# Performance work log

Hardware: AMD Instinct MI355X
Metric: run time of the kernel (lower is better)

Reference implementation:

```python
import jax, jax.numpy as jnp
import numpy as np

INPUT_DIM = 21
HIDDEN = 512
OUT_DIM = 20


def _lstm_cell(xt, h, c, Wx, bx, Wh):
    # xt: (B, in), h/c: (B, H); Wx: (4H, in), Wh: (4H, H), bx: (4H,)
    gates = xt @ Wx.T + bx + h @ Wh.T          # (B, 4H)
    i, f, g, o = jnp.split(gates, 4, axis=-1)   # torch chunk order: i, f, g, o
    i = jax.nn.sigmoid(i)
    f = jax.nn.sigmoid(f)
    g = jnp.tanh(g)
    o = jax.nn.sigmoid(o)
    c_new = f * c + i * g
    h_new = o * jnp.tanh(c_new)
    return h_new, c_new


def setup_inputs() -> dict:
    key = jax.random.key(0)
    ks = jax.random.split(key, 8)
    s_in = 1.0 / np.sqrt(INPUT_DIM)
    s_h = 1.0 / np.sqrt(HIDDEN)
    x = jax.random.normal(ks[0], (64, 1024, INPUT_DIM), dtype=jnp.float32)
    Wx0 = jax.random.uniform(ks[1], (4 * HIDDEN, INPUT_DIM), jnp.float32, -s_in, s_in)
    bx0 = jax.random.uniform(ks[2], (4 * HIDDEN,), jnp.float32, -s_in, s_in)
    Wh0 = jax.random.uniform(ks[3], (4 * HIDDEN, HIDDEN), jnp.float32, -s_h, s_h)
    Wx1 = jax.random.uniform(ks[4], (4 * HIDDEN, HIDDEN), jnp.float32, -s_h, s_h)
    bx1 = jax.random.uniform(ks[5], (4 * HIDDEN,), jnp.float32, -s_h, s_h)
    Wh1 = jax.random.uniform(ks[6], (4 * HIDDEN, HIDDEN), jnp.float32, -s_h, s_h)
    Wo = jax.random.uniform(ks[7], (OUT_DIM, HIDDEN), jnp.float32, -s_h, s_h)
    bo = jnp.zeros((OUT_DIM,), jnp.float32)
    return {"x": x, "Wx0": Wx0, "bx0": bx0, "Wh0": Wh0,
            "Wx1": Wx1, "bx1": bx1, "Wh1": Wh1, "Wo": Wo, "bo": bo}


def reference(x, Wx0, bx0, Wh0, Wx1, bx1, Wh1, Wo, bo):
    B, T, _ = x.shape
    H = Wh0.shape[1]
    h0 = jnp.zeros((B, H), x.dtype)
    c0 = jnp.zeros((B, H), x.dtype)
    h1 = jnp.zeros((B, H), x.dtype)
    c1 = jnp.zeros((B, H), x.dtype)

    def step(carry, xt):
        h0, c0, h1, c1 = carry
        h0, c0 = _lstm_cell(xt, h0, c0, Wx0, bx0, Wh0)
        h1, c1 = _lstm_cell(h0, h1, c1, Wx1, bx1, Wh1)
        out = jax.nn.sigmoid(h1 @ Wo.T + bo)  # (B, OUT_DIM)
        return (h0, c0, h1, c1), out

    _, outs = jax.lax.scan(step, (h0, c0, h1, c1), jnp.swapaxes(x, 0, 1))
    return jnp.swapaxes(outs, 0, 1)  # (B, T, OUT_DIM)
```

## Files before the change

### kernel.cpp

```cpp
#include <hip/hip_runtime.h>


#define T_STEPS 1024
#define WS_FLAG_OFF 0
#define WS_H0_OFF  4096
#define WS_H1_OFF  (4096 + 8*4*8192)
#define WS_NEED    (WS_H1_OFF + 8*2*8192)

#define SCOPE __HIP_MEMORY_SCOPE_AGENT

typedef _Float16 f16;
typedef _Float16 f16x8 __attribute__((ext_vector_type(8)));
typedef float    f32x4 __attribute__((ext_vector_type(4)));
typedef unsigned long long u64;

#define HP_STRIDE 520

__device__ __forceinline__ float sigm_(float x) {
    x = fminf(fmaxf(x, -30.f), 30.f);
    return 1.f / (1.f + __expf(-x));
}
__device__ __forceinline__ float tanh_(float x) {
    x = fminf(fmaxf(x, -15.f), 15.f);
    float e = __expf(-2.f * x);
    return (1.f - e) / (1.f + e);
}

__device__ __forceinline__ f16x8 afrag_lds(const f16* __restrict__ hp, int kbase,
                                           int b, int q) {
    return *(const f16x8*)(hp + (b & 7) * HP_STRIDE + kbase + q * 8);
}

__device__ __forceinline__ f16x8 pack8(const float* p) {
    float4 a = *(const float4*)p, b = *(const float4*)(p + 4);
    f16x8 f;
    f[0] = (f16)a.x; f[1] = (f16)a.y; f[2] = (f16)a.z; f[3] = (f16)a.w;
    f[4] = (f16)b.x; f[5] = (f16)b.y; f[6] = (f16)b.z; f[7] = (f16)b.w;
    return f;
}

__device__ __forceinline__ long long wait_flags(const int* f0, int t0,
                                                const int* f1, int t1, int lane,
                                                long long predict_clk) {
    const int* p = (lane & 16) ? (f1 + (lane & 15) * 4) : (f0 + (lane & 15) * 4);
    const int tgt = (lane & 16) ? t1 : t0;
    const bool act = (lane < 32);
    int v = act ? __hip_atomic_load(p, __ATOMIC_RELAXED, SCOPE) : 0x7fffffff;
    if (__all(v >= tgt)) return 0;
    long long t0c = (long long)__builtin_amdgcn_s_memtime();
    int rep = (int)(predict_clk >> 12);
    if (rep > 8) rep = 8;
    for (int i = 0; i < rep; ++i) __builtin_amdgcn_s_sleep(31);
    int spins = 0;
    for (;;) {
        v = act ? __hip_atomic_load(p, __ATOMIC_RELAXED, SCOPE) : 0x7fffffff;
        if (__all(v >= tgt)) break;
        ++spins;
        if (spins < 32)       __builtin_amdgcn_s_sleep(1);
        else if (spins < 256) __builtin_amdgcn_s_sleep(4);
        else                  __builtin_amdgcn_s_sleep(16);
        if (spins > (1 << 20)) break;
    }
    return (long long)__builtin_amdgcn_s_memtime() - t0c;
}

__device__ __forceinline__ long long ewma_upd(long long ew, long long d) {
    return ew - (ew >> 2) + (d >> 2);
}

__device__ __forceinline__ u64 ld8_sc0(const u64* p) {
    u64 v;
    asm volatile("global_load_dwordx2 %0, %1, off sc0" : "=v"(v) : "v"(p));
    return v;
}

__device__ __forceinline__ void stage_plane(const f16* __restrict__ gp,
                                            f16* __restrict__ dst, int tid,
                                            bool fast) {
    const u64* g8 = (const u64*)gp;
    u64 v[4];
    if (fast) {
#pragma unroll
        for (int jj = 0; jj < 4; ++jj) v[jj] = ld8_sc0(g8 + jj * 256 + tid);
        asm volatile("s_waitcnt vmcnt(0)" ::: "memory");
    } else {
#pragma unroll
        for (int jj = 0; jj < 4; ++jj)
            v[jj] = __hip_atomic_load(g8 + jj * 256 + tid, __ATOMIC_RELAXED, SCOPE);
    }
#pragma unroll
    for (int jj = 0; jj < 4; ++jj) {
        int i = jj * 256 + tid;
        int wg = i >> 6, b = (i >> 3) & 7, j = i & 7;
        *(u64*)(dst + b * HP_STRIDE + wg * 32 + j * 4) = v[jj];
    }
}

__device__ __forceinline__ void stage_two(const f16* __restrict__ gpA,
                                          f16* __restrict__ dstA,
                                          const f16* __restrict__ gpB,
                                          f16* __restrict__ dstB, int tid,
                                          bool fast) {
    const u64* ga = (const u64*)gpA;
    const u64* gb = (const u64*)gpB;
    u64 va[4], vb[4];
    if (fast) {
#pragma unroll
        for (int jj = 0; jj < 4; ++jj) va[jj] = ld8_sc0(ga + jj * 256 + tid);
#pragma unroll
        for (int jj = 0; jj < 4; ++jj) vb[jj] = ld8_sc0(gb + jj * 256 + tid);
        asm volatile("s_waitcnt vmcnt(0)" ::: "memory");
    } else {
#pragma unroll
        for (int jj = 0; jj < 4; ++jj)
            va[jj] = __hip_atomic_load(ga + jj * 256 + tid, __ATOMIC_RELAXED, SCOPE);
#pragma unroll
        for (int jj = 0; jj < 4; ++jj)
            vb[jj] = __hip_atomic_load(gb + jj * 256 + tid, __ATOMIC_RELAXED, SCOPE);
    }
#pragma unroll
    for (int jj = 0; jj < 4; ++jj) {
        int i = jj * 256 + tid;
        int wg = i >> 6, b = (i >> 3) & 7, j = i & 7;
        *(u64*)(dstA + b * HP_STRIDE + wg * 32 + j * 4) = va[jj];
        *(u64*)(dstB + b * HP_STRIDE + wg * 32 + j * 4) = vb[jj];
    }
}

__device__ __forceinline__ f16x8 load_xfrag(const float* __restrict__ x,
                                            int gb8, int t, int ln, int q) {
    f16x8 f = {(_Float16)0, (_Float16)0, (_Float16)0, (_Float16)0,
               (_Float16)0, (_Float16)0, (_Float16)0, (_Float16)0};
    if (ln < 8 && t < T_STEPS) {
        const float* xp = x + ((size_t)(gb8 + ln) * 1024 + t) * 21;
#pragma unroll
        for (int j = 0; j < 8; ++j) {
            int kl = q * 8 + j;
            if (kl < 21) f[j] = (f16)xp[kl];
        }
    }
    return f;
}

__global__ void zero_ws_kernel(unsigned* __restrict__ p, int ndw) {
    int i = blockIdx.x * blockDim.x + threadIdx.x;
    int stride = gridDim.x * blockDim.x;
    for (; i < ndw; i += stride)
        __hip_atomic_store(p + i, 0u, __ATOMIC_RELAXED, SCOPE);
}

__global__ __launch_bounds__(256, 1)
void lstm_persist(const float* __restrict__ x,
                  const float* __restrict__ Wx0, const float* __restrict__ bx0,
                  const float* __restrict__ Wh0,
                  const float* __restrict__ Wx1, const float* __restrict__ bx1,
                  const float* __restrict__ Wh1,
                  const float* __restrict__ Wo,  const float* __restrict__ bo,
                  float* __restrict__ out, char* __restrict__ ws) {
    struct SM {
        float g[4][8][33];
        float c[8][32];
        float bias[4][32];
        __align__(8)  f16 hout[8][32];
        __align__(16) f16 planeA[8 * HP_STRIDE];
        __align__(16) f16 planeB[8 * HP_STRIDE];
        char  pad[60 * 1024];
    };
    __shared__ SM sm;
    __shared__ int s_fast;
    const int tid = threadIdx.x;
    if (tid == 0x00FFFFFFu) sm.pad[0] = 1;

    const int bid  = blockIdx.x;
    const int g    = bid & 7;
    const int rk   = bid >> 3;
    const int role = rk >> 4;
    const int r    = rk & 15;
    const int w    = tid >> 6;
    const int lane = tid & 63;
    const int ln   = lane & 15;
    const int q    = lane >> 4;
    const int gb8  = g * 8;

    int* barb  = (int*)(ws + WS_FLAG_OFF) + g * 128;
    int* flag0 = barb;
    int* flag1 = barb + 64;
    f16* H0g = (f16*)(ws + WS_H0_OFF) + g * 16384;
    f16* H1g = (f16*)(ws + WS_H1_OFF) + g * 8192;

    ((float*)sm.c)[tid] = 0.f;
    if (tid < 128) {
        int gate = tid >> 5, u = tid & 31;
        const float* bx = role ? bx1 : bx0;
        sm.bias[gate][u] = bx[(gate << 9) + (r << 5) + u];
    }

    f16x8 W[64];
    if (role == 0) {
#pragma unroll
        for (int tau = 0; tau < 2; ++tau) {
            const int rw = (w << 9) + (r << 5) + tau * 16 + ln;
            const float* wh0r = Wh0 + (size_t)rw * 512;
#pragma unroll
            for (int kk = 0; kk < 16; ++kk)
                W[tau * 17 + kk] = pack8(wh0r + kk * 32 + q * 8);
            const float* wx0r = Wx0 + (size_t)rw * 21;
            f16x8 f = {(_Float16)0, (_Float16)0, (_Float16)0, (_Float16)0,
                       (_Float16)0, (_Float16)0, (_Float16)0, (_Float16)0};
#pragma unroll
            for (int j = 0; j < 8; ++j) {
                int kl = q * 8 + j;
                if (kl < 21) f[j] = (f16)wx0r[kl];
            }
            W[tau * 17 + 16] = f;
        }
    } else {
#pragma unroll
        for (int tau = 0; tau < 2; ++tau) {
            const int rw = (w << 9) + (r << 5) + tau * 16 + ln;
            const float* wx1r = Wx1 + (size_t)rw * 512;
            const float* wh1r = Wh1 + (size_t)rw * 512;
#pragma unroll
            for (int kk = 0; kk < 16; ++kk)
                W[tau * 32 + kk] = pack8(wx1r + kk * 32 + q * 8);
#pragma unroll
            for (int kk = 16; kk < 32; ++kk)
                W[tau * 32 + kk] = pack8(wh1r + (kk - 16) * 32 + q * 8);
        }
    }

    if (tid == 0) {
        unsigned xcc;
        asm volatile("s_getreg_b32 %0, hwreg(HW_REG_XCC_ID)" : "=s"(xcc));
        __hip_atomic_fetch_or(barb + 1, (int)(1u << (xcc & 31)),
                              __ATOMIC_RELAXED, SCOPE);
        __hip_atomic_fetch_add(barb + 2, 1, __ATOMIC_RELAXED, SCOPE);
        int cnt = 0, spins = 0;
        for (;;) {
            cnt = __hip_atomic_load(barb + 2, __ATOMIC_RELAXED, SCOPE);
            if (cnt >= 32 || spins > (1 << 18)) break;
            __builtin_amdgcn_s_sleep(2);
            ++spins;
        }
        unsigned m = (unsigned)__hip_atomic_load(barb + 1, __ATOMIC_RELAXED, SCOPE);
        s_fast = (cnt >= 32 && __popc(m) == 1) ? 1 : 0;
    }
    __syncthreads();
    const bool fast = (s_fast != 0);

    if (role == 0) {
        long long ew = 0;
        for (int t = 0; t < T_STEPS; ++t) {
            const int wr = t & 3, rd = (t + 3) & 3;
            f16x8 xf = load_xfrag(x, gb8, t, ln, q);
            if (tid < 64) {
                long long d = wait_flags(flag0, t, flag1, t - 3, lane, ew);
                ew = ewma_upd(ew, d);
            }
            __syncthreads();
            stage_plane(H0g + rd * 4096, sm.planeA, tid, fast);
            __syncthreads();

            f32x4 a0 = {0, 0, 0, 0}, a1 = {0, 0, 0, 0};
#pragma unroll
            for (int kk = 0; kk < 16; ++kk) {
                f16x8 A = afrag_lds(sm.planeA, kk * 32, ln, q);
                a0 = __builtin_amdgcn_mfma_f32_16x16x32_f16(A, W[kk], a0, 0, 0, 0);
                a1 = __builtin_amdgcn_mfma_f32_16x16x32_f16(A, W[17 + kk], a1, 0, 0, 0);
            }
            a0 = __builtin_amdgcn_mfma_f32_16x16x32_f16(xf, W[16], a0, 0, 0, 0);
            a1 = __builtin_amdgcn_mfma_f32_16x16x32_f16(xf, W[33], a1, 0, 0, 0);
            if (q < 2) {
#pragma unroll
                for (int r4 = 0; r4 < 4; ++r4) {
                    sm.g[w][q * 4 + r4][ln] = a0[r4];
                    sm.g[w][q * 4 + r4][16 + ln] = a1[r4];
                }
            }
            __syncthreads();
            {
                int b = tid >> 5, u = tid & 31;
                float gi = sm.g[0][b][u] + sm.bias[0][u];
                float gf = sm.g[1][b][u] + sm.bias[1][u];
                float gg = sm.g[2][b][u] + sm.bias[2][u];
                float go = sm.g[3][b][u] + sm.bias[3][u];
                float iv = sigm_(gi), fv = sigm_(gf), gv = tanh_(gg), ov = sigm_(go);
                float c = sm.c[b][u];
                float cn = fv * c + iv * gv;
                sm.c[b][u] = cn;
                sm.hout[b][u] = (f16)(ov * tanh_(cn));
            }
            __syncthreads();
            if (tid < 64) {
                int b = tid >> 3, j = tid & 7;
                u64 v = *(const u64*)&sm.hout[b][j * 4];
                u64* dp = (u64*)(H0g + wr * 4096 + (r << 8) + (b << 5) + (j << 2));
                if (fast) *dp = v;
                else __hip_atomic_store(dp, v, __ATOMIC_RELAXED, SCOPE);
                asm volatile("s_waitcnt vmcnt(0)" ::: "memory");
                if (tid == 0)
                    __hip_atomic_store(flag0 + r * 4, t + 1, __ATOMIC_RELAXED, SCOPE);
            }
        }
    } else {
        long long ew = 0;
        for (int t = 0; t < T_STEPS; ++t) {
            const int wr = t & 1, rd = wr ^ 1;

            if (tid < 64) {
                long long d = wait_flags(flag0, t + 1, flag1, t, lane, ew);
                ew = ewma_upd(ew, d);
            }
            __syncthreads();
            stage_two(H0g + (t & 3) * 4096, sm.planeA,
                      H1g + rd * 4096,      sm.planeB,
                      tid, fast);
            __syncthreads();

            f32x4 a0 = {0, 0, 0, 0}, a1 = {0, 0, 0, 0};
#pragma unroll
            for (int kk = 0; kk < 16; ++kk) {
                f16x8 A = afrag_lds(sm.planeA, kk * 32, ln, q);
                a0 = __builtin_amdgcn_mfma_f32_16x16x32_f16(A, W[kk], a0, 0, 0, 0);
                a1 = __builtin_amdgcn_mfma_f32_16x16x32_f16(A, W[32 + kk], a1, 0, 0, 0);
            }
#pragma unroll
            for (int kk = 16; kk < 32; ++kk) {
                f16x8 A = afrag_lds(sm.planeB, (kk - 16) * 32, ln, q);
                a0 = __builtin_amdgcn_mfma_f32_16x16x32_f16(A, W[kk], a0, 0, 0, 0);
                a1 = __builtin_amdgcn_mfma_f32_16x16x32_f16(A, W[32 + kk], a1, 0, 0, 0);
            }
            if (q < 2) {
#pragma unroll
                for (int r4 = 0; r4 < 4; ++r4) {
                    sm.g[w][q * 4 + r4][ln] = a0[r4];
                    sm.g[w][q * 4 + r4][16 + ln] = a1[r4];
                }
            }
            __syncthreads();
            {
                int b = tid >> 5, u = tid & 31;
                float gi = sm.g[0][b][u] + sm.bias[0][u];
                float gf = sm.g[1][b][u] + sm.bias[1][u];
                float gg = sm.g[2][b][u] + sm.bias[2][u];
                float go = sm.g[3][b][u] + sm.bias[3][u];
                float iv = sigm_(gi), fv = sigm_(gf), gv = tanh_(gg), ov = sigm_(go);
                float c = sm.c[b][u];
                float cn = fv * c + iv * gv;
                sm.c[b][u] = cn;
                sm.hout[b][u] = (f16)(ov * tanh_(cn));
            }
            __syncthreads();
            if (tid < 64) {
                int b = tid >> 3, j = tid & 7;
                u64 v = *(const u64*)&sm.hout[b][j * 4];
                u64* dp = (u64*)(H1g + wr * 4096 + (r << 8) + (b << 5) + (j << 2));
                if (fast) *dp = v;
                else __hip_atomic_store(dp, v, __ATOMIC_RELAXED, SCOPE);
                asm volatile("s_waitcnt vmcnt(0)" ::: "memory");
                if (tid == 0)
                    __hip_atomic_store(flag1 + r * 4, t + 1, __ATOMIC_RELAXED, SCOPE);
            }

            if (t > 0) {
                int p = tid >> 4, kp = tid & 15;
                int valid = (p < 10);
                int idx = r * 10 + p;
                int b = valid ? idx / 20 : 0, o = valid ? idx % 20 : 0;
                float a = 0.f;
                if (valid) {
                    const f16* hp = sm.planeB + b * HP_STRIDE + kp * 32;
                    const float* wo = Wo + (size_t)o * 512 + kp * 32;
#pragma unroll
                    for (int k = 0; k < 32; k += 8) {
                        f16x8 hv = *(const f16x8*)(hp + k);
                        float4 wa = *(const float4*)(wo + k);
                        float4 wb = *(const float4*)(wo + k + 4);
                        a += (float)hv[0] * wa.x + (float)hv[1] * wa.y +
                             (float)hv[2] * wa.z + (float)hv[3] * wa.w +
                             (float)hv[4] * wb.x + (float)hv[5] * wb.y +
                             (float)hv[6] * wb.z + (float)hv[7] * wb.w;
                    }
                }
                a += __shfl_down(a, 8, 16);
                a += __shfl_down(a, 4, 16);
                a += __shfl_down(a, 2, 16);
                a += __shfl_down(a, 1, 16);
                if (valid && kp == 0)
                    out[((size_t)(gb8 + b) * 1024 + (t - 1)) * 20 + o] =
                        sigm_(a + bo[o]);
            }
        }

        if (tid < 64) wait_flags(flag1, T_STEPS, flag1, T_STEPS, lane, 0);
        __syncthreads();
        stage_plane(H1g + ((T_STEPS - 1) & 1) * 4096, sm.planeB, tid, fast);
        __syncthreads();
        {
            int p = tid >> 4, kp = tid & 15;
            int valid = (p < 10);
            int idx = r * 10 + p;
            int b = valid ? idx / 20 : 0, o = valid ? idx % 20 : 0;
            float a = 0.f;
            if (valid) {
                const f16* hp = sm.planeB + b * HP_STRIDE + kp * 32;
                const float* wo = Wo + (size_t)o * 512 + kp * 32;
#pragma unroll
                for (int k = 0; k < 32; k += 8) {
                    f16x8 hv = *(const f16x8*)(hp + k);
                    float4 wa = *(const float4*)(wo + k);
                    float4 wb = *(const float4*)(wo + k + 4);
                    a += (float)hv[0] * wa.x + (float)hv[1] * wa.y +
                         (float)hv[2] * wa.z + (float)hv[3] * wa.w +
                         (float)hv[4] * wb.x + (float)hv[5] * wb.y +
                         (float)hv[6] * wb.z + (float)hv[7] * wb.w;
                }
            }
            a += __shfl_down(a, 8, 16);
            a += __shfl_down(a, 4, 16);
            a += __shfl_down(a, 2, 16);
            a += __shfl_down(a, 1, 16);
            if (valid && kp == 0)
                out[((size_t)(gb8 + b) * 1024 + (T_STEPS - 1)) * 20 + o] =
                    sigm_(a + bo[o]);
        }
    }
}

extern "C" void kernel_launch(void* const* d_in, const int* in_sizes, int n_in,
                              void* d_out, int out_size, void* d_ws, size_t ws_size,
                              hipStream_t stream) {
    const float* x   = (const float*)d_in[0];
    const float* Wx0 = (const float*)d_in[1];
    const float* bx0 = (const float*)d_in[2];
    const float* Wh0 = (const float*)d_in[3];
    const float* Wx1 = (const float*)d_in[4];
    const float* bx1 = (const float*)d_in[5];
    const float* Wh1 = (const float*)d_in[6];
    const float* Wo  = (const float*)d_in[7];
    const float* bo  = (const float*)d_in[8];
    float* out = (float*)d_out;
    char*  ws  = (char*)d_ws;

    if (ws_size < (size_t)WS_NEED) return;

    zero_ws_kernel<<<128, 256, 0, stream>>>((unsigned*)ws, WS_NEED / 4);
    lstm_persist<<<256, 256, 0, stream>>>(x, Wx0, bx0, Wh0, Wx1, bx1, Wh1,
                                          Wo, bo, out, ws);
}
```

Baseline: 3.439 ms.

## Precompute layer-1 input projection for next step before waiting on h1

Splits the layer-1 step so the Wx1·h0 half of the gate GEMM for step t+1 is computed right after publishing h1 for step t, as soon as layer 0's h0 is ready. At step t+1 the layer-1 blocks then only wait for h1 and do the Wh1 half, which shortens the per-step critical path on the recurrent dependency. The cost is separate flag waits and staging for each plane, extra barriers, and accumulator registers carried across iterations.

```diff
diff --git a/kernel.cpp b/kernel.cpp
--- a/kernel.cpp
+++ b/kernel.cpp
@@ -8,6 +8,7 @@
 #define WS_NEED    (WS_H1_OFF + 8*2*8192)
 
 #define SCOPE __HIP_MEMORY_SCOPE_AGENT
+#define NEG_INF_T (-1000000000)
 
 typedef _Float16 f16;
 typedef _Float16 f16x8 __attribute__((ext_vector_type(8)));
@@ -96,37 +97,6 @@
     }
 }
 
-__device__ __forceinline__ void stage_two(const f16* __restrict__ gpA,
-                                          f16* __restrict__ dstA,
-                                          const f16* __restrict__ gpB,
-                                          f16* __restrict__ dstB, int tid,
-                                          bool fast) {
-    const u64* ga = (const u64*)gpA;
-    const u64* gb = (const u64*)gpB;
-    u64 va[4], vb[4];
-    if (fast) {
-#pragma unroll
-        for (int jj = 0; jj < 4; ++jj) va[jj] = ld8_sc0(ga + jj * 256 + tid);
-#pragma unroll
-        for (int jj = 0; jj < 4; ++jj) vb[jj] = ld8_sc0(gb + jj * 256 + tid);
-        asm volatile("s_waitcnt vmcnt(0)" ::: "memory");
-    } else {
-#pragma unroll
-        for (int jj = 0; jj < 4; ++jj)
-            va[jj] = __hip_atomic_load(ga + jj * 256 + tid, __ATOMIC_RELAXED, SCOPE);
-#pragma unroll
-        for (int jj = 0; jj < 4; ++jj)
-            vb[jj] = __hip_atomic_load(gb + jj * 256 + tid, __ATOMIC_RELAXED, SCOPE);
-    }
-#pragma unroll
-    for (int jj = 0; jj < 4; ++jj) {
-        int i = jj * 256 + tid;
-        int wg = i >> 6, b = (i >> 3) & 7, j = i & 7;
-        *(u64*)(dstA + b * HP_STRIDE + wg * 32 + j * 4) = va[jj];
-        *(u64*)(dstB + b * HP_STRIDE + wg * 32 + j * 4) = vb[jj];
-    }
-}
-
 __device__ __forceinline__ f16x8 load_xfrag(const float* __restrict__ x,
                                             int gb8, int t, int ln, int q) {
     f16x8 f = {(_Float16)0, (_Float16)0, (_Float16)0, (_Float16)0,
@@ -303,27 +273,32 @@
             }
         }
     } else {
-        long long ew = 0;
+        long long ew0 = 0, ew1 = 0;
+        f32x4 pA0 = {0, 0, 0, 0}, pA1 = {0, 0, 0, 0};
+
+        if (tid < 64) wait_flags(flag0, 1, flag1, NEG_INF_T, lane, 0);
+        __syncthreads();
+        stage_plane(H0g + 0 * 4096, sm.planeA, tid, fast);
+        __syncthreads();
+#pragma unroll
+        for (int kk = 0; kk < 16; ++kk) {
+            f16x8 A = afrag_lds(sm.planeA, kk * 32, ln, q);
+            pA0 = __builtin_amdgcn_mfma_f32_16x16x32_f16(A, W[kk], pA0, 0, 0, 0);
+            pA1 = __builtin_amdgcn_mfma_f32_16x16x32_f16(A, W[32 + kk], pA1, 0, 0, 0);
+        }
+
         for (int t = 0; t < T_STEPS; ++t) {
             const int wr = t & 1, rd = wr ^ 1;
 
             if (tid < 64) {
-                long long d = wait_flags(flag0, t + 1, flag1, t, lane, ew);
-                ew = ewma_upd(ew, d);
-            }
-            __syncthreads();
-            stage_two(H0g + (t & 3) * 4096, sm.planeA,
-                      H1g + rd * 4096,      sm.planeB,
-                      tid, fast);
-            __syncthreads();
-
-            f32x4 a0 = {0, 0, 0, 0}, a1 = {0, 0, 0, 0};
-#pragma unroll
-            for (int kk = 0; kk < 16; ++kk) {
-                f16x8 A = afrag_lds(sm.planeA, kk * 32, ln, q);
-                a0 = __builtin_amdgcn_mfma_f32_16x16x32_f16(A, W[kk], a0, 0, 0, 0);
-                a1 = __builtin_amdgcn_mfma_f32_16x16x32_f16(A, W[32 + kk], a1, 0, 0, 0);
-            }
+                long long d = wait_flags(flag1, t, flag1, t, lane, ew1);
+                ew1 = ewma_upd(ew1, d);
+            }
+            __syncthreads();
+            stage_plane(H1g + rd * 4096, sm.planeB, tid, fast);
+            __syncthreads();
+
+            f32x4 a0 = pA0, a1 = pA1;
 #pragma unroll
             for (int kk = 16; kk < 32; ++kk) {
                 f16x8 A = afrag_lds(sm.planeB, (kk - 16) * 32, ln, q);
@@ -360,6 +335,25 @@
                 asm volatile("s_waitcnt vmcnt(0)" ::: "memory");
                 if (tid == 0)
                     __hip_atomic_store(flag1 + r * 4, t + 1, __ATOMIC_RELAXED, SCOPE);
+            }
+
+            if (t + 1 < T_STEPS) {
+                if (tid < 64) {
+                    long long d = wait_flags(flag0, t + 2, flag1, NEG_INF_T,
+                                             lane, ew0);
+                    ew0 = ewma_upd(ew0, d);
+                }
+                __syncthreads();
+                stage_plane(H0g + ((t + 1) & 3) * 4096, sm.planeA, tid, fast);
+                __syncthreads();
+                pA0 = (f32x4){0, 0, 0, 0};
+                pA1 = (f32x4){0, 0, 0, 0};
+#pragma unroll
+                for (int kk = 0; kk < 16; ++kk) {
+                    f16x8 A = afrag_lds(sm.planeA, kk * 32, ln, q);
+                    pA0 = __builtin_amdgcn_mfma_f32_16x16x32_f16(A, W[kk], pA0, 0, 0, 0);
+                    pA1 = __builtin_amdgcn_mfma_f32_16x16x32_f16(A, W[32 + kk], pA1, 0, 0, 0);
+                }
             }
 
             if (t > 0) {
```

Measured after the change: 4.112 ms. 1.2x slower.

## Move output projection from layer-1 blocks to layer-0 blocks with 4-deep H1 ring

Applied to the files above, without the earlier changes.

Takes the per-step output projection (sigmoid(h1·Wo^T+bo)) off the layer-1 critical path and moves it to the layer-0 blocks. Those blocks read h1 from a ring buffer that grows from 2 to 4 slots and project step t-4, then drain the last four steps after the loop. The goal is to shorten the layer-1 step, which bounds the recurrence pipeline. In exchange, layer 0 does more staging and compute per step, and the ring needs more workspace. Reading the H1 slot for step t-4 also depends on the existing flag waits to guarantee layer 1 has written it and has not yet overwritten it.

```diff
diff --git a/kernel.cpp b/kernel.cpp
--- a/kernel.cpp
+++ b/kernel.cpp
@@ -5,7 +5,7 @@
 #define WS_FLAG_OFF 0
 #define WS_H0_OFF  4096
 #define WS_H1_OFF  (4096 + 8*4*8192)
-#define WS_NEED    (WS_H1_OFF + 8*2*8192)
+#define WS_NEED    (WS_H1_OFF + 8*4*8192)
 
 #define SCOPE __HIP_MEMORY_SCOPE_AGENT
 
@@ -142,6 +142,38 @@
     return f;
 }
 
+__device__ __forceinline__ void out_proj(const f16* __restrict__ planeB,
+                                         const float* __restrict__ Wo,
+                                         const float* __restrict__ bo,
+                                         float* __restrict__ out,
+                                         int r, int gb8, int tt, int tid) {
+    int p = tid >> 4, kp = tid & 15;
+    int valid = (p < 10);
+    int idx = r * 10 + p;
+    int b = valid ? idx / 20 : 0, o = valid ? idx % 20 : 0;
+    float a = 0.f;
+    if (valid) {
+        const f16* hp = planeB + b * HP_STRIDE + kp * 32;
+        const float* wo = Wo + (size_t)o * 512 + kp * 32;
+#pragma unroll
+        for (int k = 0; k < 32; k += 8) {
+            f16x8 hv = *(const f16x8*)(hp + k);
+            float4 wa = *(const float4*)(wo + k);
+            float4 wb = *(const float4*)(wo + k + 4);
+            a += (float)hv[0] * wa.x + (float)hv[1] * wa.y +
+                 (float)hv[2] * wa.z + (float)hv[3] * wa.w +
+                 (float)hv[4] * wb.x + (float)hv[5] * wb.y +
+                 (float)hv[6] * wb.z + (float)hv[7] * wb.w;
+        }
+    }
+    a += __shfl_down(a, 8, 16);
+    a += __shfl_down(a, 4, 16);
+    a += __shfl_down(a, 2, 16);
+    a += __shfl_down(a, 1, 16);
+    if (valid && kp == 0)
+        out[((size_t)(gb8 + b) * 1024 + tt) * 20 + o] = sigm_(a + bo[o]);
+}
+
 __global__ void zero_ws_kernel(unsigned* __restrict__ p, int ndw) {
     int i = blockIdx.x * blockDim.x + threadIdx.x;
     int stride = gridDim.x * blockDim.x;
@@ -186,7 +218,7 @@
     int* flag0 = barb;
     int* flag1 = barb + 64;
     f16* H0g = (f16*)(ws + WS_H0_OFF) + g * 16384;
-    f16* H1g = (f16*)(ws + WS_H1_OFF) + g * 8192;
+    f16* H1g = (f16*)(ws + WS_H1_OFF) + g * 16384;
 
     ((float*)sm.c)[tid] = 0.f;
     if (tid < 128) {
@@ -258,7 +290,13 @@
                 ew = ewma_upd(ew, d);
             }
             __syncthreads();
-            stage_plane(H0g + rd * 4096, sm.planeA, tid, fast);
+            if (t >= 4) {
+                stage_two(H0g + rd * 4096, sm.planeA,
+                          H1g + ((t - 4) & 3) * 4096, sm.planeB,
+                          tid, fast);
+            } else {
+                stage_plane(H0g + rd * 4096, sm.planeA, tid, fast);
+            }
             __syncthreads();
 
             f32x4 a0 = {0, 0, 0, 0}, a1 = {0, 0, 0, 0};
@@ -301,11 +339,23 @@
                 if (tid == 0)
                     __hip_atomic_store(flag0 + r * 4, t + 1, __ATOMIC_RELAXED, SCOPE);
             }
+
+            if (t >= 4)
+                out_proj(sm.planeB, Wo, bo, out, r, gb8, t - 4, tid);
+        }
+
+        if (tid < 64) wait_flags(flag1, T_STEPS, flag1, T_STEPS, lane, 0);
+        __syncthreads();
+        for (int tt = T_STEPS - 4; tt < T_STEPS; ++tt) {
+            stage_plane(H1g + (tt & 3) * 4096, sm.planeB, tid, fast);
+            __syncthreads();
+            out_proj(sm.planeB, Wo, bo, out, r, gb8, tt, tid);
+            __syncthreads();
         }
     } else {
         long long ew = 0;
         for (int t = 0; t < T_STEPS; ++t) {
-            const int wr = t & 1, rd = wr ^ 1;
+            const int wr = t & 3, rd = (t - 1) & 3;
 
             if (tid < 64) {
                 long long d = wait_flags(flag0, t + 1, flag1, t, lane, ew);
@@ -361,68 +411,6 @@
                 if (tid == 0)
                     __hip_atomic_store(flag1 + r * 4, t + 1, __ATOMIC_RELAXED, SCOPE);
             }
-
-            if (t > 0) {
-                int p = tid >> 4, kp = tid & 15;
-                int valid = (p < 10);
-                int idx = r * 10 + p;
-                int b = valid ? idx / 20 : 0, o = valid ? idx % 20 : 0;
-                float a = 0.f;
-                if (valid) {
-                    const f16* hp = sm.planeB + b * HP_STRIDE + kp * 32;
-                    const float* wo = Wo + (size_t)o * 512 + kp * 32;
-#pragma unroll
-                    for (int k = 0; k < 32; k += 8) {
-                        f16x8 hv = *(const f16x8*)(hp + k);
-                        float4 wa = *(const float4*)(wo + k);
-                        float4 wb = *(const float4*)(wo + k + 4);
-                        a += (float)hv[0] * wa.x + (float)hv[1] * wa.y +
-                             (float)hv[2] * wa.z + (float)hv[3] * wa.w +
-                             (float)hv[4] * wb.x + (float)hv[5] * wb.y +
-                             (float)hv[6] * wb.z + (float)hv[7] * wb.w;
-                    }
-                }
-                a += __shfl_down(a, 8, 16);
-                a += __shfl_down(a, 4, 16);
-                a += __shfl_down(a, 2, 16);
-                a += __shfl_down(a, 1, 16);
-                if (valid && kp == 0)
-                    out[((size_t)(gb8 + b) * 1024 + (t - 1)) * 20 + o] =
-                        sigm_(a + bo[o]);
-            }
-        }
-
-        if (tid < 64) wait_flags(flag1, T_STEPS, flag1, T_STEPS, lane, 0);
-        __syncthreads();
-        stage_plane(H1g + ((T_STEPS - 1) & 1) * 4096, sm.planeB, tid, fast);
-        __syncthreads();
-        {
-            int p = tid >> 4, kp = tid & 15;
-            int valid = (p < 10);
-            int idx = r * 10 + p;
-            int b = valid ? idx / 20 : 0, o = valid ? idx % 20 : 0;
-            float a = 0.f;
-            if (valid) {
-                const f16* hp = sm.planeB + b * HP_STRIDE + kp * 32;
-                const float* wo = Wo + (size_t)o * 512 + kp * 32;
-#pragma unroll
-                for (int k = 0; k < 32; k += 8) {
-                    f16x8 hv = *(const f16x8*)(hp + k);
-                    float4 wa = *(const float4*)(wo + k);
-                    float4 wb = *(const float4*)(wo + k + 4);
-                    a += (float)hv[0] * wa.x + (float)hv[1] * wa.y +
-                         (float)hv[2] * wa.z + (float)hv[3] * wa.w +
-                         (float)hv[4] * wb.x + (float)hv[5] * wb.y +
-                         (float)hv[6] * wb.z + (float)hv[7] * wb.w;
-                }
-            }
-            a += __shfl_down(a, 8, 16);
-            a += __shfl_down(a, 4, 16);
-            a += __shfl_down(a, 2, 16);
-            a += __shfl_down(a, 1, 16);
-            if (valid && kp == 0)
-                out[((size_t)(gb8 + b) * 1024 + (T_STEPS - 1)) * 20 + o] =
-                    sigm_(a + bo[o]);
         }
     }
 }
```

Result: no change. 3.486 ms (+1.4%).
